# Kernel optimization log

Measured on AMD Instinct MI355X. Metric: run time of the kernel, lower is better.

The kernel has to match this reference:

```python
import jax, jax.numpy as jnp
import numpy as np

# Quantization constants (match init_kwargs)
A_SCALE = 0.05   # activation scale
W_SCALE = 0.01   # weight scale
A_QN, A_QP = -128, 127  # int8 activation clamp range
STRIDE = (2, 2)
PADDING = ((1, 1), (1, 1))
DILATION = (1, 1)


def setup_inputs() -> dict:
    key = jax.random.key(0)
    kx, kw = jax.random.split(key)
    # Input activations [N, C_in, H, W]
    x = jax.random.normal(kx, (32, 256, 56, 56), dtype=jnp.float32)
    # Int4 weights in [-8, 7], stored as int-valued float32 (unpacked form of weight_packed)
    w = jax.random.randint(kw, (256, 256, 3, 3), -8, 8).astype(jnp.float32)
    return {"x": x, "w": w}


def reference(x, w):
    # Activation int8 quantization: round-half-to-even (matches torch.round), clamp to [a_qn, a_qp]
    x_q = jnp.clip(jnp.round(x / A_SCALE), A_QN, A_QP)
    # Int4xInt8 GEMM over unfolded patches == conv on quantized integer values.
    # Values are small ints so fp32 accumulation is exact (|acc| <= 2304*127*8 < 2^24).
    acc = jax.lax.conv_general_dilated(
        x_q, w,
        window_strides=STRIDE,
        padding=PADDING,
        rhs_dilation=DILATION,
        dimension_numbers=("NCHW", "OIHW", "NCHW"),
    )  # [N, C_out, H_out, W_out] = [32, 256, 28, 28]
    # Dequantize: acc_int32 * (a_scale * w_scale); bias=False; out_dtype=float32
    y = acc * (A_SCALE * W_SCALE)
    return y.astype(jnp.float32)
```

## Files before the change

kernel.cpp:

```cpp
#include <hip/hip_runtime.h>
#include <stdint.h>

typedef int v4i __attribute__((ext_vector_type(4)));

#define N_IMG 32
#define C_IN 256
#define H_IN 56
#define W_IN 56
#define C_OUT 256
#define H_OUT 28
#define W_OUT 28
#define H_PAD 58
#define W_PAD 58
#define SP_TOT (N_IMG*H_OUT*W_OUT)

#define XPAD_BYTES ((size_t)N_IMG*H_PAD*W_PAD*C_IN)


__device__ __forceinline__ void glds16(const int8_t* g, int8_t* l) {
    __builtin_amdgcn_global_load_lds(
        (const __attribute__((address_space(1))) void*)g,
        (__attribute__((address_space(3))) void*)l, 16, 0, 0);
}

__global__ __launch_bounds__(256) void quant_kernel(const float* __restrict__ x,
                                                    int8_t* __restrict__ xpad) {
    __shared__ __align__(16) int8_t lraw[57344];
    __shared__ uint32_t ldsu[W_IN * 65];
    const int hp = blockIdx.x, n = blockIdx.y;
    const int t = threadIdx.x;
    int8_t* row = xpad + ((size_t)n * H_PAD + hp) * W_PAD * C_IN;

    if (hp == 0 || hp == H_PAD - 1) {
        #pragma unroll
        for (int i = 0; i < 4; ++i) {
            int idx = i * 256 + t;
            if (idx < 928) *(int4*)(row + idx * 16) = (int4){0, 0, 0, 0};
        }
        return;
    }
    const int h = hp - 1;
    const float* xrow = x + (size_t)n * (C_IN * H_IN * W_IN) + (size_t)h * W_IN;

    #pragma unroll
    for (int p = 0; p < 14; ++p) {
        const int k = p * 256 + t;
        const int c = k / 14, w4 = k - c * 14;
        glds16((const int8_t*)(xrow + (size_t)c * (H_IN * W_IN) + w4 * 4),
               lraw + k * 16);
    }
    if (t < 32) {
        int8_t* p = (t < 16) ? (row + t * 16)
                             : (row + (size_t)(W_PAD - 1) * C_IN + (t - 16) * 16);
        *(int4*)p = (int4){0, 0, 0, 0};
    }
    __syncthreads();

    const int lane = t & 63, wv = t >> 6;
    const int j = lane >> 4, w4 = lane & 15;
    const int w4c = (w4 < 14) ? w4 : 13;
    #pragma unroll
    for (int i16 = 0; i16 < 16; ++i16) {
        const int c4p = i16 * 4 + wv;
        const float4 v = *(const float4*)(lraw + ((4 * c4p + j) * 14 + w4c) * 16);
        float f[4] = {v.x, v.y, v.z, v.w};
        uint32_t u = 0;
        #pragma unroll
        for (int i = 0; i < 4; ++i) {
            float qv = rintf(f[i] * 20.0f);
            qv = fminf(fmaxf(qv, -128.0f), 127.0f);
            u |= ((uint32_t)((int)qv & 255)) << (8 * i);
        }
        uint32_t p1 = __shfl_xor(u, 16);
        uint32_t tt = (j & 1) ? (((p1 >> 8) & 0x00FF00FFu) | (u & 0xFF00FF00u))
                              : ((u & 0x00FF00FFu) | ((p1 << 8) & 0xFF00FF00u));
        uint32_t p2 = __shfl_xor(tt, 32);
        uint32_t rr = (j & 2) ? ((p2 >> 16) | (tt & 0xFFFF0000u))
                              : ((tt & 0x0000FFFFu) | (p2 << 16));
        if (w4 < 14) ldsu[(w4 * 4 + j) * 65 + c4p] = rr;
    }
    __syncthreads();

    int8_t* op = row + C_IN;
    #pragma unroll
    for (int it = 0; it < 14; ++it) {
        int idx = it * 256 + t;
        int w = idx >> 6, c4 = idx & 63;
        *(uint32_t*)(op + (size_t)w * C_IN + c4 * 4) = ldsu[w * 65 + c4];
    }
}

__global__ __launch_bounds__(256) void wq_kernel(const float* __restrict__ w,
                                                 int8_t* __restrict__ wq) {
    int idx = blockIdx.x * 256 + threadIdx.x;
    int ci  = idx & 255;
    int co  = (idx >> 8) & 255;
    int khw = idx >> 16;
    float v = w[(size_t)(co * C_IN + ci) * 9 + khw];
    wq[idx] = (int8_t)(int)rintf(v);
}

__global__ __launch_bounds__(256) void conv_kernel(const int8_t* __restrict__ xpad,
                                                   const int8_t* __restrict__ wq,
                                                   float* __restrict__ out) {
    __shared__ __align__(16) int8_t lds[32768];
    const int t = threadIdx.x;
    const int wave = t >> 6, lane = t & 63;
    const int q = lane >> 4, s = lane & 15;
    const int co_blk = blockIdx.y * 64;
    const int sp_blk = blockIdx.x * 64;

    const int rl   = t >> 4;
    const int chunk = (t & 15) ^ (rl & 15);
    const int8_t* gw = wq + (size_t)(co_blk + rl) * 256 + chunk * 16;

    const int8_t* ga[4];
    #pragma unroll
    for (int r = 0; r < 4; ++r) {
        int sp = sp_blk + r * 16 + rl;
        int n  = sp / (H_OUT * W_OUT);
        int rm = sp - n * (H_OUT * W_OUT);
        int ho = rm / W_OUT;
        int wo = rm - ho * W_OUT;
        ga[r] = xpad + ((size_t)(n * H_PAD + ho * 2) * W_PAD + wo * 2) * C_IN + chunk * 16;
    }

    const int cw = (wave >> 1) * 32;
    const int sw = (wave & 1) * 32;
    int out_base[2];
    #pragma unroll
    for (int jj = 0; jj < 2; ++jj) {
        int sp = sp_blk + sw + jj * 16 + s;
        int n  = sp / (H_OUT * W_OUT);
        int rm = sp - n * (H_OUT * W_OUT);
        int ho = rm / W_OUT;
        int wo = rm - ho * W_OUT;
        out_base[jj] = n * (C_OUT * H_OUT * W_OUT) + ho * W_OUT + wo;
    }

    v4i acc[2][2];
    #pragma unroll
    for (int i = 0; i < 2; ++i)
        #pragma unroll
        for (int jj = 0; jj < 2; ++jj)
            acc[i][jj] = (v4i){0, 0, 0, 0};

    for (int kh = 0; kh < 3; ++kh) {
        for (int kwv = 0; kwv < 3; ++kwv) {
            __syncthreads();
            const int woff = (kh * 3 + kwv) * (C_OUT * C_IN);
            const int aoff = (kh * W_PAD + kwv) * C_IN;
            #pragma unroll
            for (int r = 0; r < 4; ++r)
                glds16(gw + woff + r * 4096, lds + r * 4096 + t * 16);
            #pragma unroll
            for (int r = 0; r < 4; ++r)
                glds16(ga[r] + aoff, lds + 16384 + r * 4096 + t * 16);
            __syncthreads();

            #pragma unroll
            for (int ks = 0; ks < 4; ++ks) {
                const int st = ((ks * 4 + q) ^ s) * 16;
                v4i a[2], b[2];
                #pragma unroll
                for (int i = 0; i < 2; ++i)
                    a[i] = *(const v4i*)(lds + (cw + i * 16 + s) * 256 + st);
                #pragma unroll
                for (int jj = 0; jj < 2; ++jj)
                    b[jj] = *(const v4i*)(lds + 16384 + (sw + jj * 16 + s) * 256 + st);
                #pragma unroll
                for (int i = 0; i < 2; ++i)
                    #pragma unroll
                    for (int jj = 0; jj < 2; ++jj)
                        acc[i][jj] = __builtin_amdgcn_mfma_i32_16x16x64_i8(
                            a[i], b[jj], acc[i][jj], 0, 0, 0);
            }
        }
    }

    #pragma unroll
    for (int jj = 0; jj < 2; ++jj) {
        #pragma unroll
        for (int i = 0; i < 2; ++i) {
            const int co0 = co_blk + cw + i * 16 + q * 4;
            #pragma unroll
            for (int r = 0; r < 4; ++r) {
                out[(size_t)out_base[jj] + (size_t)(co0 + r) * (H_OUT * W_OUT)] =
                    (float)acc[i][jj][r] * 0.0005f;
            }
        }
    }
}

extern "C" void kernel_launch(void* const* d_in, const int* in_sizes, int n_in,
                              void* d_out, int out_size, void* d_ws, size_t ws_size,
                              hipStream_t stream) {
    const float* x = (const float*)d_in[0];
    const float* w = (const float*)d_in[1];
    float* out = (float*)d_out;
    int8_t* xpad = (int8_t*)d_ws;
    int8_t* wqb  = xpad + XPAD_BYTES;

    quant_kernel<<<dim3(H_PAD, N_IMG), 256, 0, stream>>>(x, xpad);
    wq_kernel<<<(9 * C_OUT * C_IN) / 256, 256, 0, stream>>>(w, wqb);
    conv_kernel<<<dim3(SP_TOT / 64, C_OUT / 64), 256, 0, stream>>>(xpad, wqb, out);
}
```

Baseline: 189.7 us.

## Double-buffer conv LDS stages over half-K chunks; read quant input directly

The conv kernel now splits each 3x3 tap into two 128-channel halves, giving 18 stages. It double-buffers them in LDS so the global-to-LDS load of the next stage overlaps the MFMA work on the current one, and it adjusts the XOR swizzle to fit 128-byte rows. The quant kernel drops its 56KB LDS staging buffer and reads float4 values straight from global memory, adding a launch-bounds occupancy hint. The aim is to hide load latency in the conv and raise quant occupancy. The cost is more barriers per tap and possibly less coalesced global reads in the quant kernel.

```diff
diff --git a/kernel.cpp b/kernel.cpp
--- a/kernel.cpp
+++ b/kernel.cpp
@@ -23,9 +23,8 @@
         (__attribute__((address_space(3))) void*)l, 16, 0, 0);
 }
 
-__global__ __launch_bounds__(256) void quant_kernel(const float* __restrict__ x,
-                                                    int8_t* __restrict__ xpad) {
-    __shared__ __align__(16) int8_t lraw[57344];
+__global__ __launch_bounds__(256, 4) void quant_kernel(const float* __restrict__ x,
+                                                       int8_t* __restrict__ xpad) {
     __shared__ uint32_t ldsu[W_IN * 65];
     const int hp = blockIdx.x, n = blockIdx.y;
     const int t = threadIdx.x;
@@ -42,19 +41,11 @@
     const int h = hp - 1;
     const float* xrow = x + (size_t)n * (C_IN * H_IN * W_IN) + (size_t)h * W_IN;
 
-    #pragma unroll
-    for (int p = 0; p < 14; ++p) {
-        const int k = p * 256 + t;
-        const int c = k / 14, w4 = k - c * 14;
-        glds16((const int8_t*)(xrow + (size_t)c * (H_IN * W_IN) + w4 * 4),
-               lraw + k * 16);
-    }
     if (t < 32) {
         int8_t* p = (t < 16) ? (row + t * 16)
                              : (row + (size_t)(W_PAD - 1) * C_IN + (t - 16) * 16);
         *(int4*)p = (int4){0, 0, 0, 0};
     }
-    __syncthreads();
 
     const int lane = t & 63, wv = t >> 6;
     const int j = lane >> 4, w4 = lane & 15;
@@ -62,7 +53,8 @@
     #pragma unroll
     for (int i16 = 0; i16 < 16; ++i16) {
         const int c4p = i16 * 4 + wv;
-        const float4 v = *(const float4*)(lraw + ((4 * c4p + j) * 14 + w4c) * 16);
+        const float4 v = *(const float4*)(xrow + (size_t)(4 * c4p + j) * (H_IN * W_IN)
+                                          + w4c * 4);
         float f[4] = {v.x, v.y, v.z, v.w};
         uint32_t u = 0;
         #pragma unroll
@@ -110,19 +102,20 @@
     const int co_blk = blockIdx.y * 64;
     const int sp_blk = blockIdx.x * 64;
 
-    const int rl   = t >> 4;
-    const int chunk = (t & 15) ^ (rl & 15);
-    const int8_t* gw = wq + (size_t)(co_blk + rl) * 256 + chunk * 16;
-
-    const int8_t* ga[4];
-    #pragma unroll
-    for (int r = 0; r < 4; ++r) {
-        int sp = sp_blk + r * 16 + rl;
+    const int r0 = t >> 3;
+    const int xch = ((t & 7) ^ (r0 & 7)) * 16;
+    const int8_t* gw2[2];
+    const int8_t* ga2[2];
+    #pragma unroll
+    for (int jj = 0; jj < 2; ++jj) {
+        const int r = r0 + jj * 32;
+        gw2[jj] = wq + (size_t)(co_blk + r) * 256 + xch;
+        int sp = sp_blk + r;
         int n  = sp / (H_OUT * W_OUT);
         int rm = sp - n * (H_OUT * W_OUT);
         int ho = rm / W_OUT;
         int wo = rm - ho * W_OUT;
-        ga[r] = xpad + ((size_t)(n * H_PAD + ho * 2) * W_PAD + wo * 2) * C_IN + chunk * 16;
+        ga2[jj] = xpad + ((size_t)(n * H_PAD + ho * 2) * W_PAD + wo * 2) * C_IN + xch;
     }
 
     const int cw = (wave >> 1) * 32;
@@ -145,37 +138,47 @@
         for (int jj = 0; jj < 2; ++jj)
             acc[i][jj] = (v4i){0, 0, 0, 0};
 
-    for (int kh = 0; kh < 3; ++kh) {
-        for (int kwv = 0; kwv < 3; ++kwv) {
-            __syncthreads();
-            const int woff = (kh * 3 + kwv) * (C_OUT * C_IN);
-            const int aoff = (kh * W_PAD + kwv) * C_IN;
-            #pragma unroll
-            for (int r = 0; r < 4; ++r)
-                glds16(gw + woff + r * 4096, lds + r * 4096 + t * 16);
-            #pragma unroll
-            for (int r = 0; r < 4; ++r)
-                glds16(ga[r] + aoff, lds + 16384 + r * 4096 + t * 16);
-            __syncthreads();
-
-            #pragma unroll
-            for (int ks = 0; ks < 4; ++ks) {
-                const int st = ((ks * 4 + q) ^ s) * 16;
-                v4i a[2], b[2];
-                #pragma unroll
-                for (int i = 0; i < 2; ++i)
-                    a[i] = *(const v4i*)(lds + (cw + i * 16 + s) * 256 + st);
+    auto stage = [&](int hk, int bufb) {
+        const int tap = hk >> 1, hf = hk & 1;
+        const int wo_ = tap * (C_OUT * C_IN) + hf * 128;
+        const int ao_ = ((tap / 3) * W_PAD + (tap % 3)) * C_IN + hf * 128;
+        int8_t* lb = lds + bufb * 16384;
+        #pragma unroll
+        for (int jj = 0; jj < 2; ++jj) {
+            glds16(gw2[jj] + wo_, lb + (t + jj * 256) * 16);
+            glds16(ga2[jj] + ao_, lb + 8192 + (t + jj * 256) * 16);
+        }
+    };
+
+    auto compute = [&](int bufb) {
+        const int8_t* lb = lds + bufb * 16384;
+        #pragma unroll
+        for (int ks = 0; ks < 2; ++ks) {
+            const int st = ((ks * 4 + q) ^ (s & 7)) * 16;
+            v4i a[2], b[2];
+            #pragma unroll
+            for (int i = 0; i < 2; ++i)
+                a[i] = *(const v4i*)(lb + (cw + i * 16 + s) * 128 + st);
+            #pragma unroll
+            for (int jj = 0; jj < 2; ++jj)
+                b[jj] = *(const v4i*)(lb + 8192 + (sw + jj * 16 + s) * 128 + st);
+            #pragma unroll
+            for (int i = 0; i < 2; ++i)
                 #pragma unroll
                 for (int jj = 0; jj < 2; ++jj)
-                    b[jj] = *(const v4i*)(lds + 16384 + (sw + jj * 16 + s) * 256 + st);
-                #pragma unroll
-                for (int i = 0; i < 2; ++i)
-                    #pragma unroll
-                    for (int jj = 0; jj < 2; ++jj)
-                        acc[i][jj] = __builtin_amdgcn_mfma_i32_16x16x64_i8(
-                            a[i], b[jj], acc[i][jj], 0, 0, 0);
-            }
-        }
+                    acc[i][jj] = __builtin_amdgcn_mfma_i32_16x16x64_i8(
+                        a[i], b[jj], acc[i][jj], 0, 0, 0);
+        }
+    };
+
+    stage(0, 0);
+    __syncthreads();
+    #pragma unroll
+    for (int hk = 0; hk < 18; ++hk) {
+        const int cb = hk & 1;
+        if (hk < 17) stage(hk + 1, cb ^ 1);
+        compute(cb);
+        if (hk < 17) __syncthreads();
     }
 
     #pragma unroll
```

New measurement: 191.2 us. About the same (+0.8%).
